# Kernel optimization log

Hardware: AMD Instinct MI355X
Metric: run time of the kernel (lower is better)

## Reference

```python
import jax, jax.numpy as jnp
import numpy as np

B, T_PAST, FUTURE_N = 128, 1024, 512
IN_F, IP, H, OUT_F = 64, 128, 256, 64


def _init(key, shape, fan_in):
    return (jax.random.uniform(key, shape, jnp.float32) * 2.0 - 1.0) / np.sqrt(fan_in).astype(np.float32)


def setup_inputs() -> dict:
    key = jax.random.key(0)
    ks = jax.random.split(key, 16)
    return {
        "x": jax.random.normal(ks[0], (B, T_PAST, IN_F), jnp.float32),
        "future_n": FUTURE_N,
        # encoder: Linear(IN_F -> IP)
        "enc_W": _init(ks[1], (IP, IN_F), IN_F),
        "enc_b": _init(ks[2], (IP,), IN_F),
        # future encoder: Linear(H -> IP)
        "fut_W": _init(ks[3], (IP, H), H),
        "fut_b": _init(ks[4], (IP,), H),
        # decoder: Linear(H -> OUT_F)
        "dec_W": _init(ks[5], (OUT_F, H), H),
        "dec_b": _init(ks[6], (OUT_F,), H),
        # past LSTMCell(IP, H)
        "pW_ih": _init(ks[7], (4 * H, IP), H),
        "pW_hh": _init(ks[8], (4 * H, H), H),
        "pb_ih": _init(ks[9], (4 * H,), H),
        "pb_hh": _init(ks[10], (4 * H,), H),
        # future LSTMCell(IP, H)
        "fW_ih": _init(ks[11], (4 * H, IP), H),
        "fW_hh": _init(ks[12], (4 * H, H), H),
        "fb_ih": _init(ks[13], (4 * H,), H),
        "fb_hh": _init(ks[14], (4 * H,), H),
    }


def _lstm_cell(xt, h, c, W_ih, W_hh, b_ih, b_hh):
    # torch LSTMCell gate order: i, f, g, o
    gates = xt @ W_ih.T + h @ W_hh.T + (b_ih + b_hh)
    i, f, g, o = jnp.split(gates, 4, axis=-1)
    c_new = jax.nn.sigmoid(f) * c + jax.nn.sigmoid(i) * jnp.tanh(g)
    h_new = jax.nn.sigmoid(o) * jnp.tanh(c_new)
    return h_new, c_new


def reference(x, future_n, enc_W, enc_b, fut_W, fut_b, dec_W, dec_b,
              pW_ih, pW_hh, pb_ih, pb_hh, fW_ih, fW_hh, fb_ih, fb_hh):
    batch = x.shape[0]
    hidden = pW_hh.shape[1]
    h0 = jnp.zeros((batch, hidden), x.dtype)
    c0 = jnp.zeros((batch, hidden), x.dtype)

    encoded = x @ enc_W.T + enc_b  # [B, T, IP]

    def past_step(carry, xt):
        h, c = carry
        h, c = _lstm_cell(xt, h, c, pW_ih, pW_hh, pb_ih, pb_hh)
        return (h, c), h

    (h, c), hs_past = jax.lax.scan(past_step, (h0, c0), jnp.swapaxes(encoded, 0, 1))

    def fut_step(carry, _):
        h, c = carry
        inp = h @ fut_W.T + fut_b
        h, c = _lstm_cell(inp, h, c, fW_ih, fW_hh, fb_ih, fb_hh)
        return (h, c), h

    _, hs_fut = jax.lax.scan(fut_step, (h, c), None, length=future_n)

    hs = jnp.concatenate([hs_past, hs_fut], axis=0)  # [T+F, B, H]
    out = jnp.swapaxes(hs, 0, 1) @ dec_W.T + dec_b  # [B, T+F, OUT_F]
    return out
```

## Files before the change

kernel.cpp:

```cpp
#include <hip/hip_runtime.h>

#define B_    128
#define TPAST 1024
#define FN    512
#define TT    1536
#define INF   64
#define IPF   128
#define HD    256
#define NG    1024
#define OUTF  64

typedef _Float16 f16;
typedef _Float16 f16x8 __attribute__((ext_vector_type(8)));
typedef _Float16 f16x4 __attribute__((ext_vector_type(4)));
typedef float    f32x4 __attribute__((ext_vector_type(4)));

template<int N> struct ic { static constexpr int value = N; };

__device__ __forceinline__ float sigm_(float x) {
  return __builtin_amdgcn_rcpf(1.f + __expf(-x));
}
__device__ __forceinline__ float tanh_(float x) {
  return 1.f - 2.f * __builtin_amdgcn_rcpf(1.f + __expf(2.f * x));
}
__device__ __forceinline__ f16x8 oload16(const f16* p) {
  f16x8 v;
  asm volatile("global_load_dwordx4 %0, %1, off\n\ts_waitcnt vmcnt(0)"
               : "=v"(v) : "v"(p));
  return v;
}

extern "C" __global__ void eprep(
    const float* __restrict__ enc_W, const float* __restrict__ enc_b,
    const float* __restrict__ fut_W, const float* __restrict__ fut_b,
    const float* __restrict__ dec_W,
    const float* __restrict__ pW_ih, const float* __restrict__ pW_hh,
    const float* __restrict__ pb_ih, const float* __restrict__ pb_hh,
    const float* __restrict__ fW_ih, const float* __restrict__ fW_hh,
    const float* __restrict__ fb_ih, const float* __restrict__ fb_hh,
    f16* __restrict__ Wp_in, float* __restrict__ bp,
    f16* __restrict__ Wp16, f16* __restrict__ Wf16,
    float* __restrict__ bf, f16* __restrict__ dW16)
{
  int stride = gridDim.x * blockDim.x;
  int gid = blockIdx.x * blockDim.x + threadIdx.x;
  for (int i = gid; i < NG * HD; i += stride) {
    int n = i >> 8, j = i & 255;
    float s = fW_hh[i];
    for (int m = 0; m < IPF; ++m) s += fW_ih[n * IPF + m] * fut_W[m * HD + j];
    Wf16[i] = (f16)s;
    Wp16[i] = (f16)pW_hh[i];
  }
  for (int i = gid; i < NG * INF; i += stride) {
    int n = i >> 6, k = i & 63;
    float s = 0.f;
    for (int m = 0; m < IPF; ++m) s += pW_ih[n * IPF + m] * enc_W[m * INF + k];
    Wp_in[i] = (f16)s;
  }
  for (int i = gid; i < OUTF * HD; i += stride) dW16[i] = (f16)dec_W[i];
  for (int n = gid; n < NG; n += stride) {
    float s1 = pb_ih[n] + pb_hh[n], s2 = fb_ih[n] + fb_hh[n];
    for (int m = 0; m < IPF; ++m) {
      s1 += pW_ih[n * IPF + m] * enc_b[m];
      s2 += fW_ih[n * IPF + m] * fut_b[m];
    }
    bp[n] = s1; bf[n] = s2;
  }
}

extern "C" __global__ __launch_bounds__(64) void epgemm(
    const float* __restrict__ x, const f16* __restrict__ Wp_in,
    const float* __restrict__ bp, f16* __restrict__ P, int t0, int Tc)
{
  int wg = blockIdx.x;
  int tl = wg >> 3, bt = wg & 7;
  int t = t0 + tl;
  int l = (int)threadIdx.x, r = l & 15, g = l >> 4;
  const float* xb = x + ((size_t)(bt * 16 + r) * TPAST + t) * INF;
  f16x8 a[2];
#pragma unroll
  for (int kk = 0; kk < 2; ++kk) {
    const float* px = xb + kk * 32 + g * 8;
    f32x4 v0 = *(const f32x4*)px;
    f32x4 v1 = *(const f32x4*)(px + 4);
#pragma unroll
    for (int e = 0; e < 4; ++e) { a[kk][e] = (f16)v0[e]; a[kk][4 + e] = (f16)v1[e]; }
  }
  for (int nt = 0; nt < 64; ++nt) {
    int n = nt * 16 + r;
    f16x8 w0 = *(const f16x8*)(Wp_in + (size_t)n * INF + g * 8);
    f16x8 w1 = *(const f16x8*)(Wp_in + (size_t)n * INF + 32 + g * 8);
    f32x4 acc = {0.f, 0.f, 0.f, 0.f};
    acc = __builtin_amdgcn_mfma_f32_16x16x32_f16(w0, a[0], acc, 0, 0, 0);
    acc = __builtin_amdgcn_mfma_f32_16x16x32_f16(w1, a[1], acc, 0, 0, 0);
    f32x4 bias4 = *(const f32x4*)&bp[nt * 16 + 4 * g];
    f16x4 hv;
#pragma unroll
    for (int e = 0; e < 4; ++e) hv[e] = (f16)(acc[e] + bias4[e]);
    int ga = nt >> 4, jhp = (nt >> 3) & 1, wc = (nt >> 1) & 3, sc = nt & 1;
    f16* Pt = P + ((size_t)(jhp * 8 + bt) * Tc + tl) * 8192;
    *(f16x4*)(Pt + ((ga * 8 + sc * 4 + wc) * 64 + l) * 4) = hv;
  }
}

extern "C" __global__ __launch_bounds__(256, 1)
void erecur(
    const f16* __restrict__ W, const f16* __restrict__ P, int pstep,
    const float* __restrict__ bias,
    f16* __restrict__ hs, f16* __restrict__ h_state, float* __restrict__ c_state,
    f16* __restrict__ Hx, unsigned int* __restrict__ flags,
    int Tc, int seq0, int init_state)
{
  __shared__ f16  Wl[512 * 96];
  __shared__ f16  hb[2][16 * 128];
  __shared__ float cb[128 * 20];
  __shared__ f16  bl[512];

  int tid = (int)threadIdx.x;
  int w = tid >> 6, l = tid & 63, r = l & 15, g = l >> 4;
  int wg = blockIdx.x;
  int bs = wg & 7, jh = wg >> 3;
  int b0 = bs * 16;
  int pwg = wg ^ 8;

  for (int nl = tid; nl < 512; nl += 256) {
    int ng = (nl >> 7) * 256 + jh * 128 + (nl & 127);
#pragma unroll
    for (int c8 = 0; c8 < 12; ++c8) {
      f16x8 v = *(const f16x8*)(W + (size_t)ng * HD + 160 + c8 * 8);
      *(f16x8*)&Wl[(nl * 96 + c8 * 8) ^ ((nl & 7) << 3)] = v;
    }
  }
  if (bias) {
    for (int i = tid; i < 512; i += 256) {
      int ng = (i >> 7) * 256 + jh * 128 + (i & 127);
      bl[i] = (f16)bias[ng];
    }
  }
  f16x8 wf[4][2][5];
#pragma unroll
  for (int ga = 0; ga < 4; ++ga)
#pragma unroll
    for (int s = 0; s < 2; ++s) {
      int ng = ga * 256 + jh * 128 + w * 32 + s * 16 + r;
#pragma unroll
      for (int kt = 0; kt < 5; ++kt)
        wf[ga][s][kt] = oload16(W + (size_t)ng * HD + kt * 32 + g * 8);
    }
  int cur0 = seq0 & 1;
  f16x8 pa[4];
  if (init_state) {
    for (int i = tid; i < 16 * 128; i += 256) {
      int b = i >> 7, jl = i & 127;
      hb[cur0][(b * 128 + jl) ^ ((b & 7) << 3)] = (f16)0.f;
    }
    for (int i = tid; i < 128 * 20; i += 256) cb[i] = 0.f;
    f16x8 z = {};
#pragma unroll
    for (int kt = 0; kt < 4; ++kt) pa[kt] = z;
  } else {
    for (int i = tid; i < 16 * 128; i += 256) {
      int b = i >> 7, jl = i & 127;
      hb[cur0][(b * 128 + jl) ^ ((b & 7) << 3)] =
          h_state[(size_t)(b0 + b) * HD + jh * 128 + jl];
    }
    for (int i = tid; i < 16 * 128; i += 256) {
      int b = i >> 7, jl = i & 127;
      cb[jl * 20 + b] = c_state[(size_t)(b0 + b) * HD + jh * 128 + jl];
    }
#pragma unroll
    for (int kt = 0; kt < 4; ++kt)
      pa[kt] = *(const f16x8*)(h_state + (size_t)(b0 + r) * HD + (jh ^ 1) * 128 + kt * 32 + g * 8);
  }
  const f16* Pw = P ? (P + (size_t)wg * Tc * pstep) : nullptr;
  f16x4 pvA[4][2], pvB[4][2];
  if (P) {
#pragma unroll
    for (int ga = 0; ga < 4; ++ga)
#pragma unroll
      for (int s = 0; s < 2; ++s)
        pvA[ga][s] = *(const f16x4*)(Pw + ((ga * 8 + s * 4 + w) * 64 + l) * 4);
  }
  __syncthreads();

  for (int tl = 0; tl < Tc; ++tl) {
    int v = seq0 + tl;

    f32x4 acc[4][2];
#pragma unroll
    for (int ga = 0; ga < 4; ++ga)
#pragma unroll
      for (int s = 0; s < 2; ++s) acc[ga][s] = f32x4{0.f, 0.f, 0.f, 0.f};

    const f16* hbc = hb[v & 1];
    auto do_kt = [&](auto ktc, f16x8 hfrag) {
      constexpr int KT = decltype(ktc)::value;
#pragma unroll
      for (int ga = 0; ga < 4; ++ga)
#pragma unroll
        for (int s = 0; s < 2; ++s) {
          if constexpr (KT < 5) {
            acc[ga][s] = __builtin_amdgcn_mfma_f32_16x16x32_f16(wf[ga][s][KT], hfrag, acc[ga][s], 0, 0, 0);
          } else {
            int nl = ga * 128 + w * 32 + s * 16 + r;
            f16x8 aw = *(const f16x8*)&Wl[(nl * 96 + (KT - 5) * 32 + g * 8) ^ ((nl & 7) << 3)];
            acc[ga][s] = __builtin_amdgcn_mfma_f32_16x16x32_f16(aw, hfrag, acc[ga][s], 0, 0, 0);
          }
        }
    };
    auto ownfrag = [&](int ktl) {
      return *(const f16x8*)&hbc[(r * 128 + ktl * 32 + g * 8) ^ ((r & 7) << 3)];
    };

    if (jh == 0) {
      do_kt(ic<0>{}, ownfrag(0)); do_kt(ic<1>{}, ownfrag(1));
      do_kt(ic<2>{}, ownfrag(2)); do_kt(ic<3>{}, ownfrag(3));
    } else {
      do_kt(ic<4>{}, ownfrag(0)); do_kt(ic<5>{}, ownfrag(1));
      do_kt(ic<6>{}, ownfrag(2)); do_kt(ic<7>{}, ownfrag(3));
    }

    if (tl > 0) {
      while (__hip_atomic_load(&flags[pwg], __ATOMIC_ACQUIRE,
                               __HIP_MEMORY_SCOPE_AGENT) < (unsigned)v)
        __builtin_amdgcn_s_sleep(1);
      const f16* HxR = Hx + ((size_t)(v & 1) * 16 + pwg) * 2048;
#pragma unroll
      for (int kt = 0; kt < 4; ++kt)
        pa[kt] = *(const f16x8*)(HxR + r * 128 + kt * 32 + g * 8);
    }
    if (P && tl + 1 < Tc) {
#pragma unroll
      for (int ga = 0; ga < 4; ++ga)
#pragma unroll
        for (int s = 0; s < 2; ++s)
          pvB[ga][s] = *(const f16x4*)(Pw + pstep + ((ga * 8 + s * 4 + w) * 64 + l) * 4);
    }
    if (jh == 0) {
      do_kt(ic<4>{}, pa[0]); do_kt(ic<5>{}, pa[1]);
      do_kt(ic<6>{}, pa[2]); do_kt(ic<7>{}, pa[3]);
    } else {
      do_kt(ic<0>{}, pa[0]); do_kt(ic<1>{}, pa[1]);
      do_kt(ic<2>{}, pa[2]); do_kt(ic<3>{}, pa[3]);
    }

    f16* hbn = hb[(v + 1) & 1];
    f16* HxW = Hx + ((size_t)((v + 1) & 1) * 16 + wg) * 2048;
#pragma unroll
    for (int s = 0; s < 2; ++s) {
      int j4 = w * 32 + s * 16 + 4 * g;
      float cold[4];
#pragma unroll
      for (int e = 0; e < 4; ++e) cold[e] = cb[(j4 + e) * 20 + r];
      f16x4 b4[4];
      if (!P) {
#pragma unroll
        for (int ga = 0; ga < 4; ++ga) b4[ga] = *(const f16x4*)&bl[ga * 128 + j4];
      }
      union { unsigned long long u; f16 h4[4]; } pk;
#pragma unroll
      for (int e = 0; e < 4; ++e) {
        float xi = acc[0][s][e], xf = acc[1][s][e], xg = acc[2][s][e], xo = acc[3][s][e];
        if (P) {
          xi += (float)pvA[0][s][e]; xf += (float)pvA[1][s][e];
          xg += (float)pvA[2][s][e]; xo += (float)pvA[3][s][e];
        } else {
          xi += (float)b4[0][e]; xf += (float)b4[1][e];
          xg += (float)b4[2][e]; xo += (float)b4[3][e];
        }
        float ii = sigm_(xi), ff = sigm_(xf), oo = sigm_(xo), gg = tanh_(xg);
        float cn = ff * cold[e] + ii * gg;
        cb[(j4 + e) * 20 + r] = cn;
        pk.h4[e] = (f16)(oo * tanh_(cn));
      }
      __hip_atomic_store((unsigned long long*)(HxW + r * 128 + j4), pk.u,
                         __ATOMIC_RELAXED, __HIP_MEMORY_SCOPE_AGENT);
      *(unsigned long long*)&hbn[(r * 128 + j4) ^ ((r & 7) << 3)] = pk.u;
    }
    __syncthreads();

    if (tid == 0)
      __hip_atomic_store(&flags[wg], (unsigned)(v + 1),
                         __ATOMIC_RELEASE, __HIP_MEMORY_SCOPE_AGENT);

    {
      int b = tid >> 4, seg = tid & 15;
      f16x8 hv = *(const f16x8*)&hbn[(b * 128 + seg * 8) ^ ((b & 7) << 3)];
      *(f16x8*)(hs + ((size_t)tl * B_ + b0 + b) * HD + jh * 128 + seg * 8) = hv;
    }
    if (P) {
#pragma unroll
      for (int ga = 0; ga < 4; ++ga)
#pragma unroll
        for (int s = 0; s < 2; ++s) pvA[ga][s] = pvB[ga][s];
      Pw += pstep;
    }
  }
  {
    const f16* hbf = hb[(seq0 + Tc) & 1];
    int b = tid >> 4, seg = tid & 15;
    f16x8 hv = *(const f16x8*)&hbf[(b * 128 + seg * 8) ^ ((b & 7) << 3)];
    *(f16x8*)(h_state + (size_t)(b0 + b) * HD + jh * 128 + seg * 8) = hv;
  }
  for (int i = tid; i < 16 * 128; i += 256) {
    int b = i >> 7, jl = i & 127;
    c_state[(size_t)(b0 + b) * HD + jh * 128 + jl] = cb[jl * 20 + b];
  }
}

extern "C" __global__ __launch_bounds__(64) void edec(
    const f16* __restrict__ hs, const f16* __restrict__ dW,
    const float* __restrict__ dec_b, float* __restrict__ out, int t0, int Tc)
{
  int wg = blockIdx.x;
  int tt = wg >> 7, b = wg & 127;
  int l = (int)threadIdx.x, r = l & 15, g = l >> 4;
  f16x8 wfr[4][8];
#pragma unroll
  for (int nt = 0; nt < 4; ++nt)
#pragma unroll
    for (int kt = 0; kt < 8; ++kt)
      wfr[nt][kt] = *(const f16x8*)(dW + (size_t)(nt * 16 + r) * HD + kt * 32 + g * 8);
  float bb[4];
#pragma unroll
  for (int nt = 0; nt < 4; ++nt) bb[nt] = dec_b[nt * 16 + r];
  f32x4 acc[2][4];
  const f32x4 zero4 = {0.f, 0.f, 0.f, 0.f};
#pragma unroll
  for (int mt = 0; mt < 2; ++mt)
#pragma unroll
    for (int nt = 0; nt < 4; ++nt) acc[mt][nt] = zero4;
#pragma unroll
  for (int mt = 0; mt < 2; ++mt)
#pragma unroll
    for (int kt = 0; kt < 8; ++kt) {
      f16x8 a = *(const f16x8*)(hs + ((size_t)(tt * 32 + mt * 16 + r) * B_ + b) * HD + kt * 32 + g * 8);
#pragma unroll
      for (int nt = 0; nt < 4; ++nt)
        acc[mt][nt] = __builtin_amdgcn_mfma_f32_16x16x32_f16(a, wfr[nt][kt], acc[mt][nt], 0, 0, 0);
    }
#pragma unroll
  for (int mt = 0; mt < 2; ++mt)
#pragma unroll
    for (int nt = 0; nt < 4; ++nt)
#pragma unroll
      for (int e = 0; e < 4; ++e) {
        int t = t0 + tt * 32 + mt * 16 + 4 * g + e;
        out[((size_t)b * TT + t) * OUTF + nt * 16 + r] = acc[mt][nt][e] + bb[nt];
      }
}

extern "C" void kernel_launch(void* const* d_in, const int* in_sizes, int n_in,
                              void* d_out, int out_size, void* d_ws, size_t ws_size,
                              hipStream_t stream)
{
  const float* x     = (const float*)d_in[0];
  const float* enc_W = (const float*)d_in[2];
  const float* enc_b = (const float*)d_in[3];
  const float* fut_W = (const float*)d_in[4];
  const float* fut_b = (const float*)d_in[5];
  const float* dec_W = (const float*)d_in[6];
  const float* dec_b = (const float*)d_in[7];
  const float* pW_ih = (const float*)d_in[8];
  const float* pW_hh = (const float*)d_in[9];
  const float* pb_ih = (const float*)d_in[10];
  const float* pb_hh = (const float*)d_in[11];
  const float* fW_ih = (const float*)d_in[12];
  const float* fW_hh = (const float*)d_in[13];
  const float* fb_ih = (const float*)d_in[14];
  const float* fb_hh = (const float*)d_in[15];
  (void)in_sizes; (void)n_in; (void)out_size;

  char* p = (char*)d_ws;
  auto alloc = [&](size_t bytes) { char* q = p; p += (bytes + 255) & ~(size_t)255; return q; };
  f16*   Wp_in = (f16*)  alloc((size_t)NG * INF * 2);
  float* bp    = (float*)alloc((size_t)NG * 4);
  f16*   Wp16  = (f16*)  alloc((size_t)NG * HD * 2);
  f16*   Wf16  = (f16*)  alloc((size_t)NG * HD * 2);
  float* bfb   = (float*)alloc((size_t)NG * 4);
  f16*   dW16  = (f16*)  alloc((size_t)OUTF * HD * 2);
  f16*   h_st  = (f16*)  alloc((size_t)B_ * HD * 2);
  float* c_st  = (float*)alloc((size_t)B_ * HD * 4);
  f16*   Hx    = (f16*)  alloc((size_t)2 * 16 * 2048 * 2);
  unsigned int* flags = (unsigned int*)alloc(64);
  size_t fixed = (size_t)(p - (char*)d_ws);

  auto need = [&](int rr) {
    size_t pp = (size_t)(rr < TPAST ? rr : TPAST) * NG * B_ * 2;
    size_t hh = (size_t)rr * B_ * HD * 2;
    return pp + hh + 4096;
  };
  size_t avail = ws_size > fixed ? ws_size - fixed : 0;
  int R = 128;
  if (avail >= need(1536)) R = 1536;
  else if (avail >= need(512)) R = 512;
  else if (avail >= need(256)) R = 256;

  f16* Pbuf = (f16*)alloc((size_t)(R < TPAST ? R : TPAST) * NG * B_ * 2);
  f16* HS   = (f16*)alloc((size_t)R * B_ * HD * 2);

  hipMemsetAsync(flags, 0, 64, stream);

  eprep<<<512, 256, 0, stream>>>(enc_W, enc_b, fut_W, fut_b, dec_W,
                                 pW_ih, pW_hh, pb_ih, pb_hh,
                                 fW_ih, fW_hh, fb_ih, fb_hh,
                                 Wp_in, bp, Wp16, Wf16, bfb, dW16);

  for (int t0 = 0; t0 < TPAST; t0 += R) {
    int Tc = (TPAST - t0) < R ? (TPAST - t0) : R;
    epgemm<<<Tc * 8, 64, 0, stream>>>(x, Wp_in, bp, Pbuf, t0, Tc);
    erecur<<<16, 256, 0, stream>>>(Wp16, Pbuf, 8192, nullptr, HS, h_st, c_st,
                                   Hx, flags, Tc, t0, t0 == 0 ? 1 : 0);
    edec<<<(Tc / 32) * B_, 64, 0, stream>>>(HS, dW16, dec_b, (float*)d_out, t0, Tc);
  }
  for (int t0 = TPAST; t0 < TT; t0 += R) {
    int Tc = (TT - t0) < R ? (TT - t0) : R;
    erecur<<<16, 256, 0, stream>>>(Wf16, nullptr, 0, bfb, HS, h_st, c_st,
                                   Hx, flags, Tc, t0, 0);
    edec<<<(Tc / 32) * B_, 64, 0, stream>>>(HS, dW16, dec_b, (float*)d_out, t0, Tc);
  }
}
```

Baseline: 6.088 ms.

## Fuse decoder projection into recurrent kernel, drop hidden-state buffer and edec

Computes the output decoder matmul inside the recurrent kernel one step late, using the previous step's local hidden slice and the partner block's exchanged half. The decoder weights live in LDS, and the hidden buffer gains a third slot so the previous state stays valid. This removes the separate edec launches and the global round trip for the hidden-state sequence. The P prefetch double-buffering is dropped in favour of a load at the start of each step. In exchange, the serial recurrence loop now does extra MFMA and global-store work each step, which can lengthen the critical path.

```diff
diff --git a/kernel.cpp b/kernel.cpp
--- a/kernel.cpp
+++ b/kernel.cpp
@@ -107,12 +107,15 @@
 void erecur(
     const f16* __restrict__ W, const f16* __restrict__ P, int pstep,
     const float* __restrict__ bias,
-    f16* __restrict__ hs, f16* __restrict__ h_state, float* __restrict__ c_state,
+    const f16* __restrict__ dW, const float* __restrict__ dec_b,
+    float* __restrict__ out,
+    f16* __restrict__ h_state, float* __restrict__ c_state,
     f16* __restrict__ Hx, unsigned int* __restrict__ flags,
-    int Tc, int seq0, int init_state)
+    int Tc, int seq0, int init_state, int do_tail)
 {
   __shared__ f16  Wl[512 * 96];
-  __shared__ f16  hb[2][16 * 128];
+  __shared__ f16  Wd[32 * 256];
+  __shared__ f16  hb[3][16 * 128];
   __shared__ float cb[128 * 20];
   __shared__ f16  bl[512];
 
@@ -131,6 +134,11 @@
       *(f16x8*)&Wl[(nl * 96 + c8 * 8) ^ ((nl & 7) << 3)] = v;
     }
   }
+  for (int i = tid; i < 32 * 32; i += 256) {
+    int row = i >> 5, c8 = i & 31;
+    f16x8 v = *(const f16x8*)(dW + (size_t)(jh * 32 + row) * HD + c8 * 8);
+    *(f16x8*)&Wd[(row * 256 + c8 * 8) ^ ((row & 7) << 3)] = v;
+  }
   if (bias) {
     for (int i = tid; i < 512; i += 256) {
       int ng = (i >> 7) * 256 + jh * 128 + (i & 127);
@@ -147,12 +155,15 @@
       for (int kt = 0; kt < 5; ++kt)
         wf[ga][s][kt] = oload16(W + (size_t)ng * HD + kt * 32 + g * 8);
     }
-  int cur0 = seq0 & 1;
+  f32x4 dbias = *(const f32x4*)(dec_b + jh * 32 + (w & 1) * 16 + 4 * g);
+  int o32 = (w & 1) * 16 + r;
+
+  int cur3 = seq0 % 3;
   f16x8 pa[4];
   if (init_state) {
     for (int i = tid; i < 16 * 128; i += 256) {
       int b = i >> 7, jl = i & 127;
-      hb[cur0][(b * 128 + jl) ^ ((b & 7) << 3)] = (f16)0.f;
+      hb[cur3][(b * 128 + jl) ^ ((b & 7) << 3)] = (f16)0.f;
     }
     for (int i = tid; i < 128 * 20; i += 256) cb[i] = 0.f;
     f16x8 z = {};
@@ -161,7 +172,7 @@
   } else {
     for (int i = tid; i < 16 * 128; i += 256) {
       int b = i >> 7, jl = i & 127;
-      hb[cur0][(b * 128 + jl) ^ ((b & 7) << 3)] =
+      hb[cur3][(b * 128 + jl) ^ ((b & 7) << 3)] =
           h_state[(size_t)(b0 + b) * HD + jh * 128 + jl];
     }
     for (int i = tid; i < 16 * 128; i += 256) {
@@ -173,26 +184,27 @@
       pa[kt] = *(const f16x8*)(h_state + (size_t)(b0 + r) * HD + (jh ^ 1) * 128 + kt * 32 + g * 8);
   }
   const f16* Pw = P ? (P + (size_t)wg * Tc * pstep) : nullptr;
-  f16x4 pvA[4][2], pvB[4][2];
-  if (P) {
-#pragma unroll
-    for (int ga = 0; ga < 4; ++ga)
-#pragma unroll
-      for (int s = 0; s < 2; ++s)
-        pvA[ga][s] = *(const f16x4*)(Pw + ((ga * 8 + s * 4 + w) * 64 + l) * 4);
-  }
   __syncthreads();
 
   for (int tl = 0; tl < Tc; ++tl) {
     int v = seq0 + tl;
-
+    int nxt3 = (cur3 + 1 == 3) ? 0 : cur3 + 1;
+
+    f16x4 pv[4][2];
+    if (P) {
+#pragma unroll
+      for (int ga = 0; ga < 4; ++ga)
+#pragma unroll
+        for (int s = 0; s < 2; ++s)
+          pv[ga][s] = *(const f16x4*)(Pw + ((ga * 8 + s * 4 + w) * 64 + l) * 4);
+    }
     f32x4 acc[4][2];
 #pragma unroll
     for (int ga = 0; ga < 4; ++ga)
 #pragma unroll
       for (int s = 0; s < 2; ++s) acc[ga][s] = f32x4{0.f, 0.f, 0.f, 0.f};
 
-    const f16* hbc = hb[v & 1];
+    const f16* hbc = hb[cur3];
     auto do_kt = [&](auto ktc, f16x8 hfrag) {
       constexpr int KT = decltype(ktc)::value;
 #pragma unroll
@@ -229,13 +241,6 @@
       for (int kt = 0; kt < 4; ++kt)
         pa[kt] = *(const f16x8*)(HxR + r * 128 + kt * 32 + g * 8);
     }
-    if (P && tl + 1 < Tc) {
-#pragma unroll
-      for (int ga = 0; ga < 4; ++ga)
-#pragma unroll
-        for (int s = 0; s < 2; ++s)
-          pvB[ga][s] = *(const f16x4*)(Pw + pstep + ((ga * 8 + s * 4 + w) * 64 + l) * 4);
-    }
     if (jh == 0) {
       do_kt(ic<4>{}, pa[0]); do_kt(ic<5>{}, pa[1]);
       do_kt(ic<6>{}, pa[2]); do_kt(ic<7>{}, pa[3]);
@@ -244,7 +249,7 @@
       do_kt(ic<2>{}, pa[2]); do_kt(ic<3>{}, pa[3]);
     }
 
-    f16* hbn = hb[(v + 1) & 1];
+    f16* hbn = hb[nxt3];
     f16* HxW = Hx + ((size_t)((v + 1) & 1) * 16 + wg) * 2048;
 #pragma unroll
     for (int s = 0; s < 2; ++s) {
@@ -262,8 +267,8 @@
       for (int e = 0; e < 4; ++e) {
         float xi = acc[0][s][e], xf = acc[1][s][e], xg = acc[2][s][e], xo = acc[3][s][e];
         if (P) {
-          xi += (float)pvA[0][s][e]; xf += (float)pvA[1][s][e];
-          xg += (float)pvA[2][s][e]; xo += (float)pvA[3][s][e];
+          xi += (float)pv[0][s][e]; xf += (float)pv[1][s][e];
+          xg += (float)pv[2][s][e]; xo += (float)pv[3][s][e];
         } else {
           xi += (float)b4[0][e]; xf += (float)b4[1][e];
           xg += (float)b4[2][e]; xo += (float)b4[3][e];
@@ -283,21 +288,67 @@
       __hip_atomic_store(&flags[wg], (unsigned)(v + 1),
                          __ATOMIC_RELEASE, __HIP_MEMORY_SCOPE_AGENT);
 
-    {
-      int b = tid >> 4, seg = tid & 15;
-      f16x8 hv = *(const f16x8*)&hbn[(b * 128 + seg * 8) ^ ((b & 7) << 3)];
-      *(f16x8*)(hs + ((size_t)tl * B_ + b0 + b) * HD + jh * 128 + seg * 8) = hv;
-    }
-    if (P) {
-#pragma unroll
-      for (int ga = 0; ga < 4; ++ga)
-#pragma unroll
-        for (int s = 0; s < 2; ++s) pvA[ga][s] = pvB[ga][s];
-      Pw += pstep;
-    }
-  }
+    if (v > 0) {
+      f32x4 dacc = {0.f, 0.f, 0.f, 0.f};
+#pragma unroll
+      for (int i = 0; i < 4; ++i) {
+        f16x8 hf = ownfrag(i);
+        int ktg = jh * 4 + i;
+        f16x8 aw = *(const f16x8*)&Wd[(o32 * 256 + ktg * 32 + g * 8) ^ ((o32 & 7) << 3)];
+        dacc = __builtin_amdgcn_mfma_f32_16x16x32_f16(aw, hf, dacc, 0, 0, 0);
+      }
+#pragma unroll
+      for (int i = 0; i < 4; ++i) {
+        int ktg = (jh ^ 1) * 4 + i;
+        f16x8 aw = *(const f16x8*)&Wd[(o32 * 256 + ktg * 32 + g * 8) ^ ((o32 & 7) << 3)];
+        dacc = __builtin_amdgcn_mfma_f32_16x16x32_f16(aw, pa[i], dacc, 0, 0, 0);
+      }
+      if (w < 2) {
+        f32x4 ov;
+#pragma unroll
+        for (int e = 0; e < 4; ++e) ov[e] = dacc[e] + dbias[e];
+        *(f32x4*)(out + ((size_t)(b0 + r) * TT + (v - 1)) * OUTF + jh * 32 + (w & 1) * 16 + 4 * g) = ov;
+      }
+    }
+
+    cur3 = nxt3;
+    if (P) Pw += pstep;
+  }
+
+  if (do_tail) {
+    while (__hip_atomic_load(&flags[pwg], __ATOMIC_ACQUIRE,
+                             __HIP_MEMORY_SCOPE_AGENT) < (unsigned)(seq0 + Tc))
+      __builtin_amdgcn_s_sleep(1);
+    const f16* HxR = Hx + ((size_t)((seq0 + Tc) & 1) * 16 + pwg) * 2048;
+    f16x8 paT[4];
+#pragma unroll
+    for (int kt = 0; kt < 4; ++kt)
+      paT[kt] = *(const f16x8*)(HxR + r * 128 + kt * 32 + g * 8);
+    const f16* hbf = hb[cur3];
+    f32x4 dacc = {0.f, 0.f, 0.f, 0.f};
+#pragma unroll
+    for (int i = 0; i < 4; ++i) {
+      f16x8 hf = *(const f16x8*)&hbf[(r * 128 + i * 32 + g * 8) ^ ((r & 7) << 3)];
+      int ktg = jh * 4 + i;
+      f16x8 aw = *(const f16x8*)&Wd[(o32 * 256 + ktg * 32 + g * 8) ^ ((o32 & 7) << 3)];
+      dacc = __builtin_amdgcn_mfma_f32_16x16x32_f16(aw, hf, dacc, 0, 0, 0);
+    }
+#pragma unroll
+    for (int i = 0; i < 4; ++i) {
+      int ktg = (jh ^ 1) * 4 + i;
+      f16x8 aw = *(const f16x8*)&Wd[(o32 * 256 + ktg * 32 + g * 8) ^ ((o32 & 7) << 3)];
+      dacc = __builtin_amdgcn_mfma_f32_16x16x32_f16(aw, paT[i], dacc, 0, 0, 0);
+    }
+    if (w < 2) {
+      f32x4 ov;
+#pragma unroll
+      for (int e = 0; e < 4; ++e) ov[e] = dacc[e] + dbias[e];
+      *(f32x4*)(out + ((size_t)(b0 + r) * TT + (seq0 + Tc - 1)) * OUTF + jh * 32 + (w & 1) * 16 + 4 * g) = ov;
+    }
+  }
+
   {
-    const f16* hbf = hb[(seq0 + Tc) & 1];
+    const f16* hbf = hb[cur3];
     int b = tid >> 4, seg = tid & 15;
     f16x8 hv = *(const f16x8*)&hbf[(b * 128 + seg * 8) ^ ((b & 7) << 3)];
     *(f16x8*)(h_state + (size_t)(b0 + b) * HD + jh * 128 + seg * 8) = hv;
@@ -306,48 +357,6 @@
     int b = i >> 7, jl = i & 127;
     c_state[(size_t)(b0 + b) * HD + jh * 128 + jl] = cb[jl * 20 + b];
   }
-}
-
-extern "C" __global__ __launch_bounds__(64) void edec(
-    const f16* __restrict__ hs, const f16* __restrict__ dW,
-    const float* __restrict__ dec_b, float* __restrict__ out, int t0, int Tc)
-{
-  int wg = blockIdx.x;
-  int tt = wg >> 7, b = wg & 127;
-  int l = (int)threadIdx.x, r = l & 15, g = l >> 4;
-  f16x8 wfr[4][8];
-#pragma unroll
-  for (int nt = 0; nt < 4; ++nt)
-#pragma unroll
-    for (int kt = 0; kt < 8; ++kt)
-      wfr[nt][kt] = *(const f16x8*)(dW + (size_t)(nt * 16 + r) * HD + kt * 32 + g * 8);
-  float bb[4];
-#pragma unroll
-  for (int nt = 0; nt < 4; ++nt) bb[nt] = dec_b[nt * 16 + r];
-  f32x4 acc[2][4];
-  const f32x4 zero4 = {0.f, 0.f, 0.f, 0.f};
-#pragma unroll
-  for (int mt = 0; mt < 2; ++mt)
-#pragma unroll
-    for (int nt = 0; nt < 4; ++nt) acc[mt][nt] = zero4;
-#pragma unroll
-  for (int mt = 0; mt < 2; ++mt)
-#pragma unroll
-    for (int kt = 0; kt < 8; ++kt) {
-      f16x8 a = *(const f16x8*)(hs + ((size_t)(tt * 32 + mt * 16 + r) * B_ + b) * HD + kt * 32 + g * 8);
-#pragma unroll
-      for (int nt = 0; nt < 4; ++nt)
-        acc[mt][nt] = __builtin_amdgcn_mfma_f32_16x16x32_f16(a, wfr[nt][kt], acc[mt][nt], 0, 0, 0);
-    }
-#pragma unroll
-  for (int mt = 0; mt < 2; ++mt)
-#pragma unroll
-    for (int nt = 0; nt < 4; ++nt)
-#pragma unroll
-      for (int e = 0; e < 4; ++e) {
-        int t = t0 + tt * 32 + mt * 16 + 4 * g + e;
-        out[((size_t)b * TT + t) * OUTF + nt * 16 + r] = acc[mt][nt][e] + bb[nt];
-      }
 }
 
 extern "C" void kernel_launch(void* const* d_in, const int* in_sizes, int n_in,
@@ -387,8 +396,7 @@
 
   auto need = [&](int rr) {
     size_t pp = (size_t)(rr < TPAST ? rr : TPAST) * NG * B_ * 2;
-    size_t hh = (size_t)rr * B_ * HD * 2;
-    return pp + hh + 4096;
+    return pp + 4096;
   };
   size_t avail = ws_size > fixed ? ws_size - fixed : 0;
   int R = 128;
@@ -397,7 +405,7 @@
   else if (avail >= need(256)) R = 256;
 
   f16* Pbuf = (f16*)alloc((size_t)(R < TPAST ? R : TPAST) * NG * B_ * 2);
-  f16* HS   = (f16*)alloc((size_t)R * B_ * HD * 2);
+  float* out = (float*)d_out;
 
   hipMemsetAsync(flags, 0, 64, stream);
 
@@ -409,14 +417,13 @@
   for (int t0 = 0; t0 < TPAST; t0 += R) {
     int Tc = (TPAST - t0) < R ? (TPAST - t0) : R;
     epgemm<<<Tc * 8, 64, 0, stream>>>(x, Wp_in, bp, Pbuf, t0, Tc);
-    erecur<<<16, 256, 0, stream>>>(Wp16, Pbuf, 8192, nullptr, HS, h_st, c_st,
-                                   Hx, flags, Tc, t0, t0 == 0 ? 1 : 0);
-    edec<<<(Tc / 32) * B_, 64, 0, stream>>>(HS, dW16, dec_b, (float*)d_out, t0, Tc);
+    erecur<<<16, 256, 0, stream>>>(Wp16, Pbuf, 8192, nullptr, dW16, dec_b, out,
+                                   h_st, c_st, Hx, flags, Tc, t0, t0 == 0 ? 1 : 0, 0);
   }
   for (int t0 = TPAST; t0 < TT; t0 += R) {
     int Tc = (TT - t0) < R ? (TT - t0) : R;
-    erecur<<<16, 256, 0, stream>>>(Wf16, nullptr, 0, bfb, HS, h_st, c_st,
-                                   Hx, flags, Tc, t0, 0);
-    edec<<<(Tc / 32) * B_, 64, 0, stream>>>(HS, dW16, dec_b, (float*)d_out, t0, Tc);
-  }
-}
+    int tail = (t0 + Tc == TT) ? 1 : 0;
+    erecur<<<16, 256, 0, stream>>>(Wf16, nullptr, 0, bfb, dW16, dec_b, out,
+                                   h_st, c_st, Hx, flags, Tc, t0, 0, tail);
+  }
+}
```

Measured after the change: 5.787 ms. 4.9% less time.
